# Optimization experiments

Hardware: AMD Instinct MI355X
Metric: run time of the kernel (lower is better)

Reference implementation:

```python
import jax, jax.numpy as jnp
import numpy as np

B, C, N = 8, 512, 2048  # batch, channels (=size), tokens


def setup_inputs() -> dict:
    key = jax.random.key(0)
    ks = jax.random.split(key, 9)
    s = 1.0 / np.sqrt(C)
    return {
        "q": jax.random.normal(ks[0], (B, C, N), dtype=jnp.float32),
        "k": jax.random.normal(ks[1], (B, C, N), dtype=jnp.float32),
        "v": jax.random.normal(ks[2], (B, C, N), dtype=jnp.float32),
        "wq": jax.random.normal(ks[3], (C, C), dtype=jnp.float32) * s,
        "bq": jax.random.normal(ks[4], (C,), dtype=jnp.float32) * s,
        "wk": jax.random.normal(ks[5], (C, C), dtype=jnp.float32) * s,
        "bk": jax.random.normal(ks[6], (C,), dtype=jnp.float32) * s,
        "wv": jax.random.normal(ks[7], (C, C), dtype=jnp.float32) * s,
        "bv": jax.random.normal(ks[8], (C,), dtype=jnp.float32) * s,
    }


def _proj(x, w, b):
    # 1x1 conv over channels: out[b,c,n] = sum_i w[c,i] x[b,i,n] + b[c]
    return jnp.einsum('ci,bin->bcn', w, x) + b[None, :, None]


def reference(q, k, v, wq, bq, wk, bk, wv, bv):
    residual = q                                   # [B, C, N]
    qp = _proj(q, wq, bq).transpose(0, 2, 1)       # [B, N, C]
    kp = _proj(k, wk, bk).transpose(0, 2, 1)       # [B, N, C]
    vp = _proj(v, wv, bv).transpose(0, 2, 1)       # [B, N, C]
    attn = jnp.einsum('bnc,bmc->bnm', qp, kp)      # raw QK^T, no scale/softmax
    out = jnp.einsum('bnm,bmc->bnc', attn, vp)     # [B, N, C]
    return out.transpose(0, 2, 1) + residual       # [B, C, N]
```

## Files before the change

### kernel.cpp

```cpp
#include <hip/hip_runtime.h>
#include <hip/hip_bf16.h>
#include <stdint.h>

#define B_ 8
#define C_ 512
#define N_ 2048

typedef __bf16 bf16_t;
typedef bf16_t bf16x8 __attribute__((ext_vector_type(8)));
typedef bf16_t bf16x4 __attribute__((ext_vector_type(4)));
typedef float f32x4 __attribute__((ext_vector_type(4)));

__global__ __launch_bounds__(256) void prep_all_kernel(
    const float* __restrict__ q, const float* __restrict__ kin,
    const float* __restrict__ vin,
    const float* __restrict__ wq, const float* __restrict__ wk,
    const float* __restrict__ wv, const float* __restrict__ bq,
    const float* __restrict__ bk,
    bf16_t* __restrict__ qT, bf16_t* __restrict__ kc, bf16_t* __restrict__ vc,
    bf16_t* __restrict__ WqT, bf16_t* __restrict__ WkT, bf16_t* __restrict__ Wvb,
    float* __restrict__ s1p, float* __restrict__ sk, float* __restrict__ sv)
{
    __shared__ bf16_t tile[64][65];
    __shared__ float red256[256];
    __shared__ float red4[4];
    const int bid = blockIdx.x;
    const int tid = threadIdx.x;

    if (bid < 2048) {
        const int b = bid >> 8;
        const int rem = bid & 255;
        const int c0 = (rem >> 5) * 64;
        const int n0 = (rem & 31) * 64;
        const float* src = q + (size_t)b * C_ * N_;
        bf16_t* dT = qT + (size_t)b * N_ * C_;
        const int cx = (tid & 15) * 4, ry = tid >> 4;
#pragma unroll
        for (int r = ry; r < 64; r += 16) {
            float4 f = *(const float4*)&src[(size_t)(c0 + r) * N_ + n0 + cx];
            tile[r][cx + 0] = (bf16_t)f.x; tile[r][cx + 1] = (bf16_t)f.y;
            tile[r][cx + 2] = (bf16_t)f.z; tile[r][cx + 3] = (bf16_t)f.w;
        }
        __syncthreads();
#pragma unroll
        for (int r = ry; r < 64; r += 16) {
            bf16x4 o;
            o[0] = tile[cx + 0][r]; o[1] = tile[cx + 1][r];
            o[2] = tile[cx + 2][r]; o[3] = tile[cx + 3][r];
            *(bf16x4*)&dT[(size_t)(n0 + r) * C_ + c0 + cx] = o;
        }
    } else if (bid < 2241) {
        const int t = bid - 2048;
        if (t < 128) {
            const float* src = (t < 64) ? wq : wk;
            bf16_t* dst = (t < 64) ? WqT : WkT;
            const int j = t & 63;
            const int i0 = (j & 7) * 64, c0 = (j >> 3) * 64;
            const int cx = (tid & 15) * 4, ry = tid >> 4;
#pragma unroll
            for (int r = ry; r < 64; r += 16) {
                float4 f = *(const float4*)&src[(size_t)(c0 + r) * C_ + i0 + cx];
                tile[r][cx + 0] = (bf16_t)f.x; tile[r][cx + 1] = (bf16_t)f.y;
                tile[r][cx + 2] = (bf16_t)f.z; tile[r][cx + 3] = (bf16_t)f.w;
            }
            __syncthreads();
#pragma unroll
            for (int r = ry; r < 64; r += 16) {
                bf16x4 o;
                o[0] = tile[cx + 0][r]; o[1] = tile[cx + 1][r];
                o[2] = tile[cx + 2][r]; o[3] = tile[cx + 3][r];
                *(bf16x4*)&dst[(size_t)(i0 + r) * C_ + c0 + cx] = o;
            }
        } else if (t < 192) {
            const int j = t - 128;
#pragma unroll
            for (int p = 0; p < 4; ++p) {
                const int i = j * 4096 + p * 1024 + tid * 4;
                float4 f = *(const float4*)(wv + i);
                bf16x4 o;
                o[0] = (bf16_t)f.x; o[1] = (bf16_t)f.y;
                o[2] = (bf16_t)f.z; o[3] = (bf16_t)f.w;
                *(bf16x4*)(Wvb + i) = o;
            }
        } else {
            float p = bk[tid] * bq[tid] + bk[tid + 256] * bq[tid + 256];
            red256[tid] = p;
            __syncthreads();
            for (int s = 128; s > 0; s >>= 1) {
                if (tid < s) red256[tid] += red256[tid + s];
                __syncthreads();
            }
            if (tid == 0) s1p[0] = red256[0];
        }
    } else {
        const int r = bid - 2241;
        const int row = r & 4095;
        const int selv = r >> 12;
        const float* src = (selv ? vin : kin) + (size_t)row * N_;
        bf16_t* dst = (selv ? vc : kc) + (size_t)row * N_;
        const int i = tid * 8;
        float4 f0 = *(const float4*)(src + i);
        float4 f1 = *(const float4*)(src + i + 4);
        bf16x8 o;
        o[0] = (bf16_t)f0.x; o[1] = (bf16_t)f0.y; o[2] = (bf16_t)f0.z; o[3] = (bf16_t)f0.w;
        o[4] = (bf16_t)f1.x; o[5] = (bf16_t)f1.y; o[6] = (bf16_t)f1.z; o[7] = (bf16_t)f1.w;
        *(bf16x8*)(dst + i) = o;
        float s = f0.x + f0.y + f0.z + f0.w + f1.x + f1.y + f1.z + f1.w;
#pragma unroll
        for (int d = 1; d < 64; d <<= 1) s += __shfl_xor(s, d, 64);
        if ((tid & 63) == 0) red4[tid >> 6] = s;
        __syncthreads();
        if (tid == 0)
            (selv ? sv : sk)[row] = red4[0] + red4[1] + red4[2] + red4[3];
    }
}

__global__ __launch_bounds__(256, 2) void dkv_M_kernel(
    const bf16_t* __restrict__ kc, const bf16_t* __restrict__ vc,
    bf16_t* __restrict__ Dp,
    const bf16_t* __restrict__ WqT, const bf16_t* __restrict__ WkT,
    bf16_t* __restrict__ M, const float* __restrict__ bq,
    const float* __restrict__ bk, float* __restrict__ gk,
    float* __restrict__ va)
{
    __shared__ __align__(16) bf16_t As[128 * 64];
    __shared__ __align__(16) bf16_t Bs[128 * 64];
    const int f = blockIdx.x;
    const int tid = threadIdx.x, lane = tid & 63, wave = tid >> 6;
    const int wr = wave >> 1, wc = wave & 1;
    const size_t sCC = (size_t)C_ * C_;
    const size_t sBN = (size_t)N_ * C_;

    if (f < 512) {
        const int zz = f >> 4;
        const int bz = zz >> 2, sp = zz & 3;
        const int t4 = f & 15;
        const int m0 = (t4 >> 2) * 128, n0 = (t4 & 3) * 128;
        const int kbeg = sp * 512;
        const bf16_t* Ab = kc + (size_t)bz * sBN;
        const bf16_t* Bb = vc + (size_t)bz * sBN;

        f32x4 acc[4][4];
#pragma unroll
        for (int i = 0; i < 4; ++i)
#pragma unroll
            for (int j = 0; j < 4; ++j) acc[i][j] = 0.f;

        const int srow = tid >> 3;
        const int scol = ((tid & 7) ^ (srow & 7)) * 8;
        const int ldso = tid * 16;

        for (int t = 0; t < 8; ++t) {
            const bf16_t* ga = Ab + (size_t)(m0 + srow) * N_ + kbeg + t * 64 + scol;
            const bf16_t* gb = Bb + (size_t)(n0 + srow) * N_ + kbeg + t * 64 + scol;
#pragma unroll
            for (int p = 0; p < 4; ++p)
                __builtin_amdgcn_global_load_lds(
                    (const __attribute__((address_space(1))) void*)(ga + (size_t)p * 32 * N_),
                    (__attribute__((address_space(3))) void*)((char*)As + ldso + p * 4096),
                    16, 0, 0);
#pragma unroll
            for (int p = 0; p < 4; ++p)
                __builtin_amdgcn_global_load_lds(
                    (const __attribute__((address_space(1))) void*)(gb + (size_t)p * 32 * N_),
                    (__attribute__((address_space(3))) void*)((char*)Bs + ldso + p * 4096),
                    16, 0, 0);
            __syncthreads();

#pragma unroll
            for (int kk = 0; kk < 64; kk += 32) {
                bf16x8 af[4], bfr[4];
                const int kcol = kk + (lane >> 4) * 8;
                const int kcn = kcol >> 3;
#pragma unroll
                for (int m = 0; m < 4; ++m) {
                    const int r = wr * 64 + (lane & 15) + m * 16;
                    af[m] = *(const bf16x8*)((const char*)As + r * 128 +
                                             ((kcn ^ (r & 7)) << 4));
                }
#pragma unroll
                for (int n = 0; n < 4; ++n) {
                    const int r = wc * 64 + (lane & 15) + n * 16;
                    bfr[n] = *(const bf16x8*)((const char*)Bs + r * 128 +
                                              ((kcn ^ (r & 7)) << 4));
                }
#pragma unroll
                for (int m = 0; m < 4; ++m)
#pragma unroll
                    for (int n = 0; n < 4; ++n)
                        acc[m][n] = __builtin_amdgcn_mfma_f32_16x16x32_bf16(
                            af[m], bfr[n], acc[m][n], 0, 0, 0);
            }
            __syncthreads();
        }

        const int rj = (lane >> 4) * 4;
        const int cc = lane & 15;
#pragma unroll
        for (int m = 0; m < 4; ++m)
#pragma unroll
            for (int n = 0; n < 4; ++n) {
                const int col = n0 + wc * 64 + n * 16 + cc;
                f32x4 vv = acc[m][n];
#pragma unroll
                for (int j = 0; j < 4; ++j) {
                    const int row = m0 + wr * 64 + m * 16 + rj + j;
                    Dp[(size_t)zz * sCC + (size_t)row * C_ + col] = (bf16_t)vv[j];
                }
            }
    } else if (f < 576) {
        const int g = f - 512;
        const int m0 = (g >> 3) * 64, n0 = (g & 7) * 64;
        f32x4 acc[2][2];
#pragma unroll
        for (int i = 0; i < 2; ++i)
#pragma unroll
            for (int j = 0; j < 2; ++j) acc[i][j] = 0.f;
        const int srow = tid >> 3;
        const int scol = ((tid & 7) ^ (srow & 7)) * 8;
        const int ldso = tid * 16;
        for (int t = 0; t < 8; ++t) {
            const bf16_t* ga = WqT + (size_t)(m0 + srow) * C_ + t * 64 + scol;
            const bf16_t* gb = WkT + (size_t)(n0 + srow) * C_ + t * 64 + scol;
#pragma unroll
            for (int p = 0; p < 2; ++p)
                __builtin_amdgcn_global_load_lds(
                    (const __attribute__((address_space(1))) void*)(ga + (size_t)p * 32 * C_),
                    (__attribute__((address_space(3))) void*)((char*)As + ldso + p * 4096),
                    16, 0, 0);
#pragma unroll
            for (int p = 0; p < 2; ++p)
                __builtin_amdgcn_global_load_lds(
                    (const __attribute__((address_space(1))) void*)(gb + (size_t)p * 32 * C_),
                    (__attribute__((address_space(3))) void*)((char*)Bs + ldso + p * 4096),
                    16, 0, 0);
            __syncthreads();
#pragma unroll
            for (int kk = 0; kk < 64; kk += 32) {
                bf16x8 af[2], bfr[2];
                const int kcol = kk + (lane >> 4) * 8;
                const int kcn = kcol >> 3;
#pragma unroll
                for (int m = 0; m < 2; ++m) {
                    const int r = wr * 32 + (lane & 15) + m * 16;
                    af[m] = *(const bf16x8*)((const char*)As + r * 128 +
                                             ((kcn ^ (r & 7)) << 4));
                }
#pragma unroll
                for (int n = 0; n < 2; ++n) {
                    const int r = wc * 32 + (lane & 15) + n * 16;
                    bfr[n] = *(const bf16x8*)((const char*)Bs + r * 128 +
                                              ((kcn ^ (r & 7)) << 4));
                }
#pragma unroll
                for (int m = 0; m < 2; ++m)
#pragma unroll
                    for (int n = 0; n < 2; ++n)
                        acc[m][n] = __builtin_amdgcn_mfma_f32_16x16x32_bf16(
                            af[m], bfr[n], acc[m][n], 0, 0, 0);
            }
            __syncthreads();
        }
        const int rj = (lane >> 4) * 4;
        const int cc = lane & 15;
#pragma unroll
        for (int m = 0; m < 2; ++m)
#pragma unroll
            for (int n = 0; n < 2; ++n) {
                const int col = n0 + wc * 32 + n * 16 + cc;
                f32x4 vv = acc[m][n];
#pragma unroll
                for (int j = 0; j < 4; ++j) {
                    const int row = m0 + wr * 32 + m * 16 + rj + j;
                    M[(size_t)row * C_ + col] = (bf16_t)vv[j];
                }
            }
    } else {
        const int j = f - 576;
        const bf16_t* W = (j < 8) ? WkT : WqT;
        const float* bb = (j < 8) ? bq : bk;
        float* out = (j < 8) ? gk : va;
        const int row = (j & 7) * 64 + (tid >> 2);
        const int c0 = (tid & 3) * 128;
        const bf16_t* rp = W + (size_t)row * C_ + c0;
        float acc = 0.f;
#pragma unroll
        for (int e = 0; e < 128; e += 8) {
            bf16x8 vv = *(const bf16x8*)(rp + e);
#pragma unroll
            for (int x = 0; x < 8; ++x) acc += (float)vv[x] * bb[c0 + e + x];
        }
        acc += __shfl_xor(acc, 1, 64);
        acc += __shfl_xor(acc, 2, 64);
        if ((tid & 3) == 0) out[row] = acc;
    }
}

__global__ __launch_bounds__(256) void p1_fused_kernel(
    const bf16_t* __restrict__ Wvb, const bf16_t* __restrict__ Dp,
    bf16_t* __restrict__ P1, const bf16_t* __restrict__ M,
    const float* __restrict__ sk, const float* __restrict__ sv,
    const float* __restrict__ gk, const float* __restrict__ s1p,
    float* __restrict__ u, float* __restrict__ vbraw, float* __restrict__ s2)
{
    __shared__ __align__(16) bf16_t As[64 * 64];
    __shared__ __align__(16) bf16_t Bs[64 * 64];
    __shared__ float svec[C_];
    __shared__ float red[256];
    const int f = blockIdx.x;
    const int tid = threadIdx.x, lane = tid & 63, wave = tid >> 6;
    const int wr = wave >> 1, wc = wave & 1;
    const size_t sCC = (size_t)C_ * C_;

    if (f < 512) {
        const int bz = f >> 6;
        const int m0 = ((f >> 3) & 7) * 64, n0 = (f & 7) * 64;
        f32x4 acc[2][2];
#pragma unroll
        for (int i = 0; i < 2; ++i)
#pragma unroll
            for (int j = 0; j < 2; ++j) acc[i][j] = 0.f;
        const int srow = tid >> 3;
        const int scol = ((tid & 7) ^ (srow & 7)) * 8;
        const int ldso = tid * 16;

        for (int sp = 0; sp < 4; ++sp) {
            const bf16_t* Bb = Dp + (size_t)(bz * 4 + sp) * sCC;
            for (int t = 0; t < 8; ++t) {
                const bf16_t* ga = Wvb + (size_t)(m0 + srow) * C_ + t * 64 + scol;
                const bf16_t* gb = Bb + (size_t)(n0 + srow) * C_ + t * 64 + scol;
#pragma unroll
                for (int p = 0; p < 2; ++p)
                    __builtin_amdgcn_global_load_lds(
                        (const __attribute__((address_space(1))) void*)(ga + (size_t)p * 32 * C_),
                        (__attribute__((address_space(3))) void*)((char*)As + ldso + p * 4096),
                        16, 0, 0);
#pragma unroll
                for (int p = 0; p < 2; ++p)
                    __builtin_amdgcn_global_load_lds(
                        (const __attribute__((address_space(1))) void*)(gb + (size_t)p * 32 * C_),
                        (__attribute__((address_space(3))) void*)((char*)Bs + ldso + p * 4096),
                        16, 0, 0);
                __syncthreads();
#pragma unroll
                for (int kk = 0; kk < 64; kk += 32) {
                    bf16x8 af[2], bfr[2];
                    const int kcol = kk + (lane >> 4) * 8;
                    const int kcn = kcol >> 3;
#pragma unroll
                    for (int m = 0; m < 2; ++m) {
                        const int r = wr * 32 + (lane & 15) + m * 16;
                        af[m] = *(const bf16x8*)((const char*)As + r * 128 +
                                                 ((kcn ^ (r & 7)) << 4));
                    }
#pragma unroll
                    for (int n = 0; n < 2; ++n) {
                        const int r = wc * 32 + (lane & 15) + n * 16;
                        bfr[n] = *(const bf16x8*)((const char*)Bs + r * 128 +
                                                  ((kcn ^ (r & 7)) << 4));
                    }
#pragma unroll
                    for (int m = 0; m < 2; ++m)
#pragma unroll
                        for (int n = 0; n < 2; ++n)
                            acc[m][n] = __builtin_amdgcn_mfma_f32_16x16x32_bf16(
                                af[m], bfr[n], acc[m][n], 0, 0, 0);
                }
                __syncthreads();
            }
        }
        const int rj = (lane >> 4) * 4;
        const int cc = lane & 15;
#pragma unroll
        for (int m = 0; m < 2; ++m)
#pragma unroll
            for (int n = 0; n < 2; ++n) {
                const int col = n0 + wc * 32 + n * 16 + cc;
                f32x4 vv = acc[m][n];
#pragma unroll
                for (int j = 0; j < 4; ++j) {
                    const int row = m0 + wr * 32 + m * 16 + rj + j;
                    P1[(size_t)bz * sCC + (size_t)row * C_ + col] = (bf16_t)vv[j];
                }
            }
    } else if (f < 520) {
        const int b = f - 512;
        const float* s4 = sv + (size_t)b * C_;
        svec[tid * 2] = s4[tid * 2];
        svec[tid * 2 + 1] = s4[tid * 2 + 1];
        __syncthreads();
        const int c = tid * 2;
#pragma unroll
        for (int rr = 0; rr < 2; ++rr) {
            const bf16_t* row = Wvb + (size_t)(c + rr) * C_;
            float acc = 0.f;
            for (int j = 0; j < C_; j += 8) {
                bf16x8 vv = *(const bf16x8*)(row + j);
#pragma unroll
                for (int e = 0; e < 8; ++e) acc += (float)vv[e] * svec[j + e];
            }
            u[b * C_ + c + rr] = acc;
        }
    } else {
        const int b = f - 520;
        const float* s4 = sk + (size_t)b * C_;
        svec[tid * 2] = s4[tid * 2];
        svec[tid * 2 + 1] = s4[tid * 2 + 1];
        __syncthreads();
        const int c = tid * 2;
#pragma unroll
        for (int rr = 0; rr < 2; ++rr) {
            const bf16_t* row = M + (size_t)(c + rr) * C_;
            float acc = 0.f;
            for (int j = 0; j < C_; j += 8) {
                bf16x8 vv = *(const bf16x8*)(row + j);
#pragma unroll
                for (int e = 0; e < 8; ++e) acc += (float)vv[e] * svec[j + e];
            }
            vbraw[b * C_ + c + rr] = acc;
        }
        float p = svec[tid] * gk[tid] + svec[tid + 256] * gk[tid + 256];
        red[tid] = p;
        __syncthreads();
        for (int s = 128; s > 0; s >>= 1) {
            if (tid < s) red[tid] += red[tid + s];
            __syncthreads();
        }
        if (tid == 0) s2[b] = red[0] + 2048.0f * s1p[0];
    }
}

__global__ __launch_bounds__(256) void gemm_ht(
    const bf16_t* __restrict__ A, const bf16_t* __restrict__ Bm,
    bf16_t* __restrict__ Cout,
    const float* __restrict__ e0, const float* __restrict__ e1,
    const float* __restrict__ e2, const float* __restrict__ e3,
    const float* __restrict__ bqv, float* __restrict__ hout,
    const float* __restrict__ s1p, const float* __restrict__ s2p)
{
    __shared__ __align__(16) bf16_t As[64 * 64];
    __shared__ __align__(16) bf16_t Bs[64 * 64];

    const int tid = threadIdx.x, lane = tid & 63, wave = tid >> 6;
    const int wr = wave >> 1, wc = wave & 1;
    const int bz = blockIdx.z;
    const int m0 = blockIdx.y * 64, n0 = blockIdx.x * 64;
    const size_t sCC = (size_t)C_ * C_;

    const bf16_t* Ab = A + (size_t)bz * sCC;

    f32x4 acc[2][2];
#pragma unroll
    for (int i = 0; i < 2; ++i)
#pragma unroll
        for (int j = 0; j < 2; ++j) acc[i][j] = 0.f;

    const int srow = tid >> 3;
    const int scol = ((tid & 7) ^ (srow & 7)) * 8;
    const int ldso = tid * 16;

    float hacc = 0.f;
    const bool doH = (blockIdx.x == 0);

    for (int t = 0; t < 8; ++t) {
        const bf16_t* ga = Ab + (size_t)(m0 + srow) * C_ + t * 64 + scol;
        const bf16_t* gb = Bm + (size_t)(n0 + srow) * C_ + t * 64 + scol;
#pragma unroll
        for (int p = 0; p < 2; ++p)
            __builtin_amdgcn_global_load_lds(
                (const __attribute__((address_space(1))) void*)(ga + (size_t)p * 32 * C_),
                (__attribute__((address_space(3))) void*)((char*)As + ldso + p * 4096),
                16, 0, 0);
#pragma unroll
        for (int p = 0; p < 2; ++p)
            __builtin_amdgcn_global_load_lds(
                (const __attribute__((address_space(1))) void*)(gb + (size_t)p * 32 * C_),
                (__attribute__((address_space(3))) void*)((char*)Bs + ldso + p * 4096),
                16, 0, 0);
        __syncthreads();

#pragma unroll
        for (int kk = 0; kk < 64; kk += 32) {
            bf16x8 af[2], bfr[2];
            const int kcol = kk + (lane >> 4) * 8;
            const int kcn = kcol >> 3;
#pragma unroll
            for (int m = 0; m < 2; ++m) {
                const int r = wr * 32 + (lane & 15) + m * 16;
                af[m] = *(const bf16x8*)((const char*)As + r * 128 +
                                         ((kcn ^ (r & 7)) << 4));
            }
#pragma unroll
            for (int n = 0; n < 2; ++n) {
                const int r = wc * 32 + (lane & 15) + n * 16;
                bfr[n] = *(const bf16x8*)((const char*)Bs + r * 128 +
                                          ((kcn ^ (r & 7)) << 4));
            }
#pragma unroll
            for (int m = 0; m < 2; ++m)
#pragma unroll
                for (int n = 0; n < 2; ++n)
                    acc[m][n] = __builtin_amdgcn_mfma_f32_16x16x32_bf16(
                        af[m], bfr[n], acc[m][n], 0, 0, 0);
        }
        if (doH) {
            const int rr = tid >> 2, qq = tid & 3;
#pragma unroll
            for (int uq = 0; uq < 2; ++uq) {
                const int c = qq * 2 + uq;
                bf16x8 av = *(const bf16x8*)((const char*)As + rr * 128 +
                                             ((c ^ (rr & 7)) << 4));
                const float* bp = bqv + t * 64 + c * 8;
#pragma unroll
                for (int e = 0; e < 8; ++e) hacc += (float)av[e] * bp[e];
            }
        }
        __syncthreads();
    }

    const int rj = (lane >> 4) * 4;
    const int cc = lane & 15;
#pragma unroll
    for (int m = 0; m < 2; ++m) {
#pragma unroll
        for (int n = 0; n < 2; ++n) {
            const int col = n0 + wc * 32 + n * 16 + cc;
            f32x4 vv = acc[m][n];
#pragma unroll
            for (int j = 0; j < 4; ++j) {
                const int row = m0 + wr * 32 + m * 16 + rj + j;
                float val = vv[j] + e0[bz * C_ + row] * e1[col] +
                            e2[row] * (e3[bz * C_ + col] + 2048.0f * e1[col]);
                Cout[(size_t)bz * sCC + (size_t)row * C_ + col] = (bf16_t)val;
            }
        }
    }
    if (doH) {
        hacc += __shfl_xor(hacc, 1, 64);
        hacc += __shfl_xor(hacc, 2, 64);
        if ((tid & 3) == 0) {
            const int row = m0 + (tid >> 2);
            hout[bz * C_ + row] = hacc + e0[bz * C_ + row] * s1p[0] +
                                  e2[row] * s2p[bz];
        }
    }
}

__global__ __launch_bounds__(256) void gemm_final(
    const bf16_t* __restrict__ A, const bf16_t* __restrict__ Bm,
    float* __restrict__ Cout, const float* __restrict__ qres,
    const float* __restrict__ hvec)
{
    __shared__ __align__(16) bf16_t As[128 * 64];
    __shared__ __align__(16) bf16_t Bs[128 * 64];

    const int f = blockIdx.x;
    const int xcd = f & 7, sl = f >> 3;
    const int g = xcd + 8 * (sl >> 2);
    const int m0 = (sl & 3) * 128;
    const int bz = g >> 4;
    const int n0 = (g & 15) * 128;
    const int K = C_;

    const int tid = threadIdx.x, lane = tid & 63, wave = tid >> 6;
    const int wr = wave >> 1, wc = wave & 1;

    const bf16_t* Ab = A + (size_t)bz * ((size_t)C_ * C_);
    const bf16_t* Bb = Bm + (size_t)bz * ((size_t)N_ * C_);

    f32x4 acc[4][4];
#pragma unroll
    for (int i = 0; i < 4; ++i)
#pragma unroll
        for (int j = 0; j < 4; ++j) acc[i][j] = 0.f;

    const int srow = tid >> 3;
    const int scol = ((tid & 7) ^ (srow & 7)) * 8;
    const int ldso = tid * 16;

    for (int t = 0; t < 8; ++t) {
        const bf16_t* ga = Ab + (size_t)(m0 + srow) * K + t * 64 + scol;
        const bf16_t* gb = Bb + (size_t)(n0 + srow) * K + t * 64 + scol;
#pragma unroll
        for (int p = 0; p < 4; ++p)
            __builtin_amdgcn_global_load_lds(
                (const __attribute__((address_space(1))) void*)(ga + (size_t)p * 32 * K),
                (__attribute__((address_space(3))) void*)((char*)As + ldso + p * 4096),
                16, 0, 0);
#pragma unroll
        for (int p = 0; p < 4; ++p)
            __builtin_amdgcn_global_load_lds(
                (const __attribute__((address_space(1))) void*)(gb + (size_t)p * 32 * K),
                (__attribute__((address_space(3))) void*)((char*)Bs + ldso + p * 4096),
                16, 0, 0);
        __syncthreads();

#pragma unroll
        for (int kk = 0; kk < 64; kk += 32) {
            bf16x8 af[4], bfr[4];
            const int kcol = kk + (lane >> 4) * 8;
            const int kcn = kcol >> 3;
#pragma unroll
            for (int m = 0; m < 4; ++m) {
                const int r = wr * 64 + (lane & 15) + m * 16;
                af[m] = *(const bf16x8*)((const char*)As + r * 128 +
                                         ((kcn ^ (r & 7)) << 4));
            }
#pragma unroll
            for (int n = 0; n < 4; ++n) {
                const int r = wc * 64 + (lane & 15) + n * 16;
                bfr[n] = *(const bf16x8*)((const char*)Bs + r * 128 +
                                          ((kcn ^ (r & 7)) << 4));
            }
#pragma unroll
            for (int m = 0; m < 4; ++m)
#pragma unroll
                for (int n = 0; n < 4; ++n)
                    acc[m][n] = __builtin_amdgcn_mfma_f32_16x16x32_bf16(
                        af[m], bfr[n], acc[m][n], 0, 0, 0);
        }
        __syncthreads();
    }

    const int rj = (lane >> 4) * 4;
    const int cc = lane & 15;
    const size_t ob = (size_t)bz * ((size_t)C_ * N_);
#pragma unroll
    for (int m = 0; m < 4; ++m) {
#pragma unroll
        for (int n = 0; n < 4; ++n) {
            const int col = n0 + wc * 64 + n * 16 + cc;
            f32x4 vv = acc[m][n];
#pragma unroll
            for (int j = 0; j < 4; ++j) {
                const int row = m0 + wr * 64 + m * 16 + rj + j;
                const size_t o = ob + (size_t)row * N_ + col;
                Cout[o] = vv[j] + hvec[bz * C_ + row] + qres[o];
            }
        }
    }
}

extern "C" void kernel_launch(void* const* d_in, const int* in_sizes, int n_in,
                              void* d_out, int out_size, void* d_ws, size_t ws_size,
                              hipStream_t stream)
{
    (void)in_sizes; (void)n_in; (void)out_size; (void)ws_size;
    const float* q  = (const float*)d_in[0];
    const float* k  = (const float*)d_in[1];
    const float* v  = (const float*)d_in[2];
    const float* wq = (const float*)d_in[3];
    const float* bq = (const float*)d_in[4];
    const float* wk = (const float*)d_in[5];
    const float* bk = (const float*)d_in[6];
    const float* wv = (const float*)d_in[7];
    const float* bv = (const float*)d_in[8];
    float* out = (float*)d_out;

    char* ws = (char*)d_ws;
    const size_t WSZ = (size_t)C_ * C_ * 2;
    const size_t TSZ = (size_t)B_ * N_ * C_ * 2;
    const size_t SCZ = (size_t)B_ * C_ * C_ * 2;
    const size_t VSZ = (size_t)B_ * C_ * 4;
    const size_t sCC = (size_t)C_ * C_;
    size_t off = 0;
    bf16_t* WqTb = (bf16_t*)(ws + off); off += WSZ;
    bf16_t* WkTb = (bf16_t*)(ws + off); off += WSZ;
    bf16_t* Wvb  = (bf16_t*)(ws + off); off += WSZ;
    bf16_t* M    = (bf16_t*)(ws + off); off += WSZ;
    bf16_t* qT   = (bf16_t*)(ws + off); off += TSZ;
    bf16_t* kc   = (bf16_t*)(ws + off); off += TSZ;
    bf16_t* vc   = (bf16_t*)(ws + off); off += TSZ;
    bf16_t* Dp   = (bf16_t*)(ws + off); off += TSZ;
    bf16_t* P1   = (bf16_t*)(ws + off); off += SCZ;
    bf16_t* HT   = (bf16_t*)(ws + off); off += SCZ;
    float*  sk   = (float*)(ws + off);  off += VSZ;
    float*  sv   = (float*)(ws + off);  off += VSZ;
    float*  gk   = (float*)(ws + off);  off += C_ * 4;
    float*  va   = (float*)(ws + off);  off += C_ * 4;
    float*  s1p  = (float*)(ws + off);  off += 64;
    float*  s2   = (float*)(ws + off);  off += 64;
    float*  uu   = (float*)(ws + off);  off += VSZ;
    float*  vbr  = (float*)(ws + off);  off += VSZ;
    float*  hb   = (float*)(ws + off);  off += VSZ;

    const dim3 blk(256);

    prep_all_kernel<<<dim3(10433), blk, 0, stream>>>(
        q, k, v, wq, wk, wv, bq, bk, qT, kc, vc, WqTb, WkTb, Wvb, s1p, sk, sv);

    dkv_M_kernel<<<dim3(592), blk, 0, stream>>>(
        kc, vc, Dp, WqTb, WkTb, M, bq, bk, gk, va);

    p1_fused_kernel<<<dim3(528), blk, 0, stream>>>(
        Wvb, Dp, P1, M, sk, sv, gk, s1p, uu, vbr, s2);

    gemm_ht<<<dim3(8, 8, B_), blk, 0, stream>>>(
        P1, M, HT, uu, va, bv, vbr, gk, hb, s1p, s2);

    gemm_final<<<dim3(512), blk, 0, stream>>>(HT, qT, out, q, hb);
}
```

Before: 111.2 us.

## Fuse K/V fp32-to-bf16 conversion and row sums into the K·V^T GEMM

Removes the separate prep pass that converted k and v to bf16 and computed their row sums. The Dk·v GEMM now loads fp32 tiles straight into LDS and converts to bf16 while building MFMA fragments. Edge blocks accumulate per-split partial row sums, which the next kernel adds up. This cuts a full read and write of two large bf16 intermediates, but doubles LDS footprint and global load volume inside the GEMM and drops the occupancy-2 launch bound. Blocks are also remapped across XCDs.

```diff
diff --git a/kernel.cpp b/kernel.cpp
--- a/kernel.cpp
+++ b/kernel.cpp
@@ -11,19 +11,17 @@
 typedef bf16_t bf16x4 __attribute__((ext_vector_type(4)));
 typedef float f32x4 __attribute__((ext_vector_type(4)));
 
-__global__ __launch_bounds__(256) void prep_all_kernel(
-    const float* __restrict__ q, const float* __restrict__ kin,
-    const float* __restrict__ vin,
+__global__ __launch_bounds__(256) void prep_qw_kernel(
+    const float* __restrict__ q,
     const float* __restrict__ wq, const float* __restrict__ wk,
     const float* __restrict__ wv, const float* __restrict__ bq,
     const float* __restrict__ bk,
-    bf16_t* __restrict__ qT, bf16_t* __restrict__ kc, bf16_t* __restrict__ vc,
+    bf16_t* __restrict__ qT,
     bf16_t* __restrict__ WqT, bf16_t* __restrict__ WkT, bf16_t* __restrict__ Wvb,
-    float* __restrict__ s1p, float* __restrict__ sk, float* __restrict__ sv)
+    float* __restrict__ s1p)
 {
     __shared__ bf16_t tile[64][65];
     __shared__ float red256[256];
-    __shared__ float red4[4];
     const int bid = blockIdx.x;
     const int tid = threadIdx.x;
 
@@ -49,96 +47,75 @@
             o[2] = tile[cx + 2][r]; o[3] = tile[cx + 3][r];
             *(bf16x4*)&dT[(size_t)(n0 + r) * C_ + c0 + cx] = o;
         }
-    } else if (bid < 2241) {
+    } else if (bid < 2176) {
         const int t = bid - 2048;
-        if (t < 128) {
-            const float* src = (t < 64) ? wq : wk;
-            bf16_t* dst = (t < 64) ? WqT : WkT;
-            const int j = t & 63;
-            const int i0 = (j & 7) * 64, c0 = (j >> 3) * 64;
-            const int cx = (tid & 15) * 4, ry = tid >> 4;
-#pragma unroll
-            for (int r = ry; r < 64; r += 16) {
-                float4 f = *(const float4*)&src[(size_t)(c0 + r) * C_ + i0 + cx];
-                tile[r][cx + 0] = (bf16_t)f.x; tile[r][cx + 1] = (bf16_t)f.y;
-                tile[r][cx + 2] = (bf16_t)f.z; tile[r][cx + 3] = (bf16_t)f.w;
-            }
+        const float* src = (t < 64) ? wq : wk;
+        bf16_t* dst = (t < 64) ? WqT : WkT;
+        const int j = t & 63;
+        const int i0 = (j & 7) * 64, c0 = (j >> 3) * 64;
+        const int cx = (tid & 15) * 4, ry = tid >> 4;
+#pragma unroll
+        for (int r = ry; r < 64; r += 16) {
+            float4 f = *(const float4*)&src[(size_t)(c0 + r) * C_ + i0 + cx];
+            tile[r][cx + 0] = (bf16_t)f.x; tile[r][cx + 1] = (bf16_t)f.y;
+            tile[r][cx + 2] = (bf16_t)f.z; tile[r][cx + 3] = (bf16_t)f.w;
+        }
+        __syncthreads();
+#pragma unroll
+        for (int r = ry; r < 64; r += 16) {
+            bf16x4 o;
+            o[0] = tile[cx + 0][r]; o[1] = tile[cx + 1][r];
+            o[2] = tile[cx + 2][r]; o[3] = tile[cx + 3][r];
+            *(bf16x4*)&dst[(size_t)(i0 + r) * C_ + c0 + cx] = o;
+        }
+    } else if (bid < 2240) {
+        const int j = bid - 2176;
+#pragma unroll
+        for (int p = 0; p < 4; ++p) {
+            const int i = j * 4096 + p * 1024 + tid * 4;
+            float4 f = *(const float4*)(wv + i);
+            bf16x4 o;
+            o[0] = (bf16_t)f.x; o[1] = (bf16_t)f.y;
+            o[2] = (bf16_t)f.z; o[3] = (bf16_t)f.w;
+            *(bf16x4*)(Wvb + i) = o;
+        }
+    } else {
+        float p = bk[tid] * bq[tid] + bk[tid + 256] * bq[tid + 256];
+        red256[tid] = p;
+        __syncthreads();
+        for (int s = 128; s > 0; s >>= 1) {
+            if (tid < s) red256[tid] += red256[tid + s];
             __syncthreads();
-#pragma unroll
-            for (int r = ry; r < 64; r += 16) {
-                bf16x4 o;
-                o[0] = tile[cx + 0][r]; o[1] = tile[cx + 1][r];
-                o[2] = tile[cx + 2][r]; o[3] = tile[cx + 3][r];
-                *(bf16x4*)&dst[(size_t)(i0 + r) * C_ + c0 + cx] = o;
-            }
-        } else if (t < 192) {
-            const int j = t - 128;
-#pragma unroll
-            for (int p = 0; p < 4; ++p) {
-                const int i = j * 4096 + p * 1024 + tid * 4;
-                float4 f = *(const float4*)(wv + i);
-                bf16x4 o;
-                o[0] = (bf16_t)f.x; o[1] = (bf16_t)f.y;
-                o[2] = (bf16_t)f.z; o[3] = (bf16_t)f.w;
-                *(bf16x4*)(Wvb + i) = o;
-            }
-        } else {
-            float p = bk[tid] * bq[tid] + bk[tid + 256] * bq[tid + 256];
-            red256[tid] = p;
-            __syncthreads();
-            for (int s = 128; s > 0; s >>= 1) {
-                if (tid < s) red256[tid] += red256[tid + s];
-                __syncthreads();
-            }
-            if (tid == 0) s1p[0] = red256[0];
-        }
-    } else {
-        const int r = bid - 2241;
-        const int row = r & 4095;
-        const int selv = r >> 12;
-        const float* src = (selv ? vin : kin) + (size_t)row * N_;
-        bf16_t* dst = (selv ? vc : kc) + (size_t)row * N_;
-        const int i = tid * 8;
-        float4 f0 = *(const float4*)(src + i);
-        float4 f1 = *(const float4*)(src + i + 4);
-        bf16x8 o;
-        o[0] = (bf16_t)f0.x; o[1] = (bf16_t)f0.y; o[2] = (bf16_t)f0.z; o[3] = (bf16_t)f0.w;
-        o[4] = (bf16_t)f1.x; o[5] = (bf16_t)f1.y; o[6] = (bf16_t)f1.z; o[7] = (bf16_t)f1.w;
-        *(bf16x8*)(dst + i) = o;
-        float s = f0.x + f0.y + f0.z + f0.w + f1.x + f1.y + f1.z + f1.w;
-#pragma unroll
-        for (int d = 1; d < 64; d <<= 1) s += __shfl_xor(s, d, 64);
-        if ((tid & 63) == 0) red4[tid >> 6] = s;
-        __syncthreads();
-        if (tid == 0)
-            (selv ? sv : sk)[row] = red4[0] + red4[1] + red4[2] + red4[3];
+        }
+        if (tid == 0) s1p[0] = red256[0];
     }
 }
 
-__global__ __launch_bounds__(256, 2) void dkv_M_kernel(
-    const bf16_t* __restrict__ kc, const bf16_t* __restrict__ vc,
-    bf16_t* __restrict__ Dp,
+__global__ __launch_bounds__(256) void dkv_M_kernel(
+    const float* __restrict__ Kin, const float* __restrict__ Vin,
+    bf16_t* __restrict__ Dp, float* __restrict__ sk4, float* __restrict__ sv4,
     const bf16_t* __restrict__ WqT, const bf16_t* __restrict__ WkT,
     bf16_t* __restrict__ M, const float* __restrict__ bq,
     const float* __restrict__ bk, float* __restrict__ gk,
     float* __restrict__ va)
 {
-    __shared__ __align__(16) bf16_t As[128 * 64];
-    __shared__ __align__(16) bf16_t Bs[128 * 64];
+    __shared__ __align__(16) float AsF[128 * 64];
+    __shared__ __align__(16) float BsF[128 * 64];
+
     const int f = blockIdx.x;
     const int tid = threadIdx.x, lane = tid & 63, wave = tid >> 6;
     const int wr = wave >> 1, wc = wave & 1;
     const size_t sCC = (size_t)C_ * C_;
-    const size_t sBN = (size_t)N_ * C_;
 
     if (f < 512) {
-        const int zz = f >> 4;
-        const int bz = zz >> 2, sp = zz & 3;
-        const int t4 = f & 15;
-        const int m0 = (t4 >> 2) * 128, n0 = (t4 & 3) * 128;
+        const int xcd = f & 7, sl = f >> 3;
+        const int g = xcd + 8 * (sl >> 4), t5 = sl & 15;
+        const int bz = g >> 2, sp = g & 3;
+        const int m0 = (t5 >> 2) * 128, n0 = (t5 & 3) * 128;
         const int kbeg = sp * 512;
-        const bf16_t* Ab = kc + (size_t)bz * sBN;
-        const bf16_t* Bb = vc + (size_t)bz * sBN;
+
+        const float* Ab = Kin + (size_t)bz * C_ * N_;
+        const float* Bb = Vin + (size_t)bz * C_ * N_;
 
         f32x4 acc[4][4];
 #pragma unroll
@@ -146,24 +123,28 @@
 #pragma unroll
             for (int j = 0; j < 4; ++j) acc[i][j] = 0.f;
 
-        const int srow = tid >> 3;
-        const int scol = ((tid & 7) ^ (srow & 7)) * 8;
+        const int prow = tid >> 4;
+        const int cs   = (tid & 15) ^ (prow & 7);
         const int ldso = tid * 16;
 
+        const int srr = tid >> 1, hh = tid & 1;
+        float hsA = 0.f, hsB = 0.f;
+        const bool doA = (n0 == 0), doB = (m0 == 0);
+
         for (int t = 0; t < 8; ++t) {
-            const bf16_t* ga = Ab + (size_t)(m0 + srow) * N_ + kbeg + t * 64 + scol;
-            const bf16_t* gb = Bb + (size_t)(n0 + srow) * N_ + kbeg + t * 64 + scol;
-#pragma unroll
-            for (int p = 0; p < 4; ++p)
+            const float* ga = Ab + (size_t)(m0 + prow) * N_ + kbeg + t * 64 + cs * 4;
+            const float* gb = Bb + (size_t)(n0 + prow) * N_ + kbeg + t * 64 + cs * 4;
+#pragma unroll
+            for (int p = 0; p < 8; ++p)
                 __builtin_amdgcn_global_load_lds(
-                    (const __attribute__((address_space(1))) void*)(ga + (size_t)p * 32 * N_),
-                    (__attribute__((address_space(3))) void*)((char*)As + ldso + p * 4096),
+                    (const __attribute__((address_space(1))) void*)(ga + (size_t)p * 16 * N_),
+                    (__attribute__((address_space(3))) void*)((char*)AsF + ldso + p * 4096),
                     16, 0, 0);
 #pragma unroll
-            for (int p = 0; p < 4; ++p)
+            for (int p = 0; p < 8; ++p)
                 __builtin_amdgcn_global_load_lds(
-                    (const __attribute__((address_space(1))) void*)(gb + (size_t)p * 32 * N_),
-                    (__attribute__((address_space(3))) void*)((char*)Bs + ldso + p * 4096),
+                    (const __attribute__((address_space(1))) void*)(gb + (size_t)p * 16 * N_),
+                    (__attribute__((address_space(3))) void*)((char*)BsF + ldso + p * 4096),
                     16, 0, 0);
             __syncthreads();
 
@@ -171,18 +152,30 @@
             for (int kk = 0; kk < 64; kk += 32) {
                 bf16x8 af[4], bfr[4];
                 const int kcol = kk + (lane >> 4) * 8;
-                const int kcn = kcol >> 3;
+                const int c1 = kcol >> 2;
 #pragma unroll
                 for (int m = 0; m < 4; ++m) {
                     const int r = wr * 64 + (lane & 15) + m * 16;
-                    af[m] = *(const bf16x8*)((const char*)As + r * 128 +
-                                             ((kcn ^ (r & 7)) << 4));
+                    f32x4 lo = *(const f32x4*)((const char*)AsF + r * 256 + ((c1 ^ (r & 7)) << 4));
+                    f32x4 hi = *(const f32x4*)((const char*)AsF + r * 256 + (((c1 + 1) ^ (r & 7)) << 4));
+                    bf16x8 fr;
+                    fr[0] = (bf16_t)lo[0]; fr[1] = (bf16_t)lo[1];
+                    fr[2] = (bf16_t)lo[2]; fr[3] = (bf16_t)lo[3];
+                    fr[4] = (bf16_t)hi[0]; fr[5] = (bf16_t)hi[1];
+                    fr[6] = (bf16_t)hi[2]; fr[7] = (bf16_t)hi[3];
+                    af[m] = fr;
                 }
 #pragma unroll
                 for (int n = 0; n < 4; ++n) {
                     const int r = wc * 64 + (lane & 15) + n * 16;
-                    bfr[n] = *(const bf16x8*)((const char*)Bs + r * 128 +
-                                              ((kcn ^ (r & 7)) << 4));
+                    f32x4 lo = *(const f32x4*)((const char*)BsF + r * 256 + ((c1 ^ (r & 7)) << 4));
+                    f32x4 hi = *(const f32x4*)((const char*)BsF + r * 256 + (((c1 + 1) ^ (r & 7)) << 4));
+                    bf16x8 fr;
+                    fr[0] = (bf16_t)lo[0]; fr[1] = (bf16_t)lo[1];
+                    fr[2] = (bf16_t)lo[2]; fr[3] = (bf16_t)lo[3];
+                    fr[4] = (bf16_t)hi[0]; fr[5] = (bf16_t)hi[1];
+                    fr[6] = (bf16_t)hi[2]; fr[7] = (bf16_t)hi[3];
+                    bfr[n] = fr;
                 }
 #pragma unroll
                 for (int m = 0; m < 4; ++m)
@@ -191,11 +184,29 @@
                         acc[m][n] = __builtin_amdgcn_mfma_f32_16x16x32_bf16(
                             af[m], bfr[n], acc[m][n], 0, 0, 0);
             }
+
+            if (doA) {
+#pragma unroll
+                for (int u = 0; u < 8; ++u) {
+                    const int slot = ((hh * 8 + u) + srr) & 15;
+                    f32x4 vv = *(const f32x4*)((const char*)AsF + srr * 256 + slot * 16);
+                    hsA += vv[0] + vv[1] + vv[2] + vv[3];
+                }
+            }
+            if (doB) {
+#pragma unroll
+                for (int u = 0; u < 8; ++u) {
+                    const int slot = ((hh * 8 + u) + srr) & 15;
+                    f32x4 vv = *(const f32x4*)((const char*)BsF + srr * 256 + slot * 16);
+                    hsB += vv[0] + vv[1] + vv[2] + vv[3];
+                }
+            }
             __syncthreads();
         }
 
         const int rj = (lane >> 4) * 4;
         const int cc = lane & 15;
+        const int z = bz * 4 + sp;
 #pragma unroll
         for (int m = 0; m < 4; ++m)
 #pragma unroll
@@ -205,10 +216,20 @@
 #pragma unroll
                 for (int j = 0; j < 4; ++j) {
                     const int row = m0 + wr * 64 + m * 16 + rj + j;
-                    Dp[(size_t)zz * sCC + (size_t)row * C_ + col] = (bf16_t)vv[j];
-                }
-            }
+                    Dp[(size_t)z * sCC + (size_t)row * C_ + col] = (bf16_t)vv[j];
+                }
+            }
+        if (doA) {
+            hsA += __shfl_xor(hsA, 1, 64);
+            if (!hh) sk4[(size_t)(sp * B_ + bz) * C_ + m0 + srr] = hsA;
+        }
+        if (doB) {
+            hsB += __shfl_xor(hsB, 1, 64);
+            if (!hh) sv4[(size_t)(sp * B_ + bz) * C_ + n0 + srr] = hsB;
+        }
     } else if (f < 576) {
+        bf16_t* As = (bf16_t*)AsF;
+        bf16_t* Bs = (bf16_t*)BsF;
         const int g = f - 512;
         const int m0 = (g >> 3) * 64, n0 = (g & 7) * 64;
         f32x4 acc[2][2];
@@ -299,7 +320,7 @@
 __global__ __launch_bounds__(256) void p1_fused_kernel(
     const bf16_t* __restrict__ Wvb, const bf16_t* __restrict__ Dp,
     bf16_t* __restrict__ P1, const bf16_t* __restrict__ M,
-    const float* __restrict__ sk, const float* __restrict__ sv,
+    const float* __restrict__ sk4, const float* __restrict__ sv4,
     const float* __restrict__ gk, const float* __restrict__ s1p,
     float* __restrict__ u, float* __restrict__ vbraw, float* __restrict__ s2)
 {
@@ -311,6 +332,7 @@
     const int tid = threadIdx.x, lane = tid & 63, wave = tid >> 6;
     const int wr = wave >> 1, wc = wave & 1;
     const size_t sCC = (size_t)C_ * C_;
+    const size_t st = (size_t)B_ * C_;
 
     if (f < 512) {
         const int bz = f >> 6;
@@ -385,9 +407,12 @@
             }
     } else if (f < 520) {
         const int b = f - 512;
-        const float* s4 = sv + (size_t)b * C_;
-        svec[tid * 2] = s4[tid * 2];
-        svec[tid * 2 + 1] = s4[tid * 2 + 1];
+        const float* s4 = sv4 + (size_t)b * C_;
+#pragma unroll
+        for (int rr = 0; rr < 2; ++rr) {
+            const int j = tid * 2 + rr;
+            svec[j] = s4[j] + s4[st + j] + s4[2 * st + j] + s4[3 * st + j];
+        }
         __syncthreads();
         const int c = tid * 2;
 #pragma unroll
@@ -403,9 +428,12 @@
         }
     } else {
         const int b = f - 520;
-        const float* s4 = sk + (size_t)b * C_;
-        svec[tid * 2] = s4[tid * 2];
-        svec[tid * 2 + 1] = s4[tid * 2 + 1];
+        const float* s4 = sk4 + (size_t)b * C_;
+#pragma unroll
+        for (int rr = 0; rr < 2; ++rr) {
+            const int j = tid * 2 + rr;
+            svec[j] = s4[j] + s4[st + j] + s4[2 * st + j] + s4[3 * st + j];
+        }
         __syncthreads();
         const int c = tid * 2;
 #pragma unroll
@@ -662,20 +690,17 @@
     const size_t TSZ = (size_t)B_ * N_ * C_ * 2;
     const size_t SCZ = (size_t)B_ * C_ * C_ * 2;
     const size_t VSZ = (size_t)B_ * C_ * 4;
-    const size_t sCC = (size_t)C_ * C_;
     size_t off = 0;
     bf16_t* WqTb = (bf16_t*)(ws + off); off += WSZ;
     bf16_t* WkTb = (bf16_t*)(ws + off); off += WSZ;
     bf16_t* Wvb  = (bf16_t*)(ws + off); off += WSZ;
     bf16_t* M    = (bf16_t*)(ws + off); off += WSZ;
     bf16_t* qT   = (bf16_t*)(ws + off); off += TSZ;
-    bf16_t* kc   = (bf16_t*)(ws + off); off += TSZ;
-    bf16_t* vc   = (bf16_t*)(ws + off); off += TSZ;
     bf16_t* Dp   = (bf16_t*)(ws + off); off += TSZ;
     bf16_t* P1   = (bf16_t*)(ws + off); off += SCZ;
     bf16_t* HT   = (bf16_t*)(ws + off); off += SCZ;
-    float*  sk   = (float*)(ws + off);  off += VSZ;
-    float*  sv   = (float*)(ws + off);  off += VSZ;
+    float*  sk4  = (float*)(ws + off);  off += 4 * VSZ;
+    float*  sv4  = (float*)(ws + off);  off += 4 * VSZ;
     float*  gk   = (float*)(ws + off);  off += C_ * 4;
     float*  va   = (float*)(ws + off);  off += C_ * 4;
     float*  s1p  = (float*)(ws + off);  off += 64;
@@ -686,14 +711,14 @@
 
     const dim3 blk(256);
 
-    prep_all_kernel<<<dim3(10433), blk, 0, stream>>>(
-        q, k, v, wq, wk, wv, bq, bk, qT, kc, vc, WqTb, WkTb, Wvb, s1p, sk, sv);
+    prep_qw_kernel<<<dim3(2241), blk, 0, stream>>>(
+        q, wq, wk, wv, bq, bk, qT, WqTb, WkTb, Wvb, s1p);
 
     dkv_M_kernel<<<dim3(592), blk, 0, stream>>>(
-        kc, vc, Dp, WqTb, WkTb, M, bq, bk, gk, va);
+        k, v, Dp, sk4, sv4, WqTb, WkTb, M, bq, bk, gk, va);
 
     p1_fused_kernel<<<dim3(528), blk, 0, stream>>>(
-        Wvb, Dp, P1, M, sk, sv, gk, s1p, uu, vbr, s2);
+        Wvb, Dp, P1, M, sk4, sv4, gk, s1p, uu, vbr, s2);
 
     gemm_ht<<<dim3(8, 8, B_), blk, 0, stream>>>(
         P1, M, HT, uu, va, bv, vbr, gk, hb, s1p, s2);
```

Result: faster. 102.7 us (median of 2 runs) (-7.7%).
